# Kernel optimization log

Hardware: AMD Instinct MI355X
Metric: run time of the kernel (lower is better)

## Reference

```python
import jax, jax.numpy as jnp
import numpy as np

# Static DAG: input -> L hidden layers of K nodes (dense between layers) -> output.
B, WIDTH, K, L = 262144, 64, 4, 4


def _linear_init(key, shape, fan_in):
    # matches nn.Linear default: U(-1/sqrt(fan_in), 1/sqrt(fan_in))
    bound = 1.0 / np.sqrt(fan_in)
    return jax.random.uniform(key, shape, jnp.float32, -bound, bound)


def setup_inputs() -> dict:
    key = jax.random.key(0)
    ks = jax.random.split(key, 9)
    x = jax.random.normal(ks[0], (B, WIDTH), jnp.float32)
    # input node -> first hidden layer (K edges)
    W_in = _linear_init(ks[1], (K, WIDTH, WIDTH), WIDTH)
    b_in = _linear_init(ks[2], (K, WIDTH), WIDTH)
    # between hidden layers: (L-1) transitions, K*K edges each; [pred, node, out, in]
    W_mid = _linear_init(ks[3], (L - 1, K, K, WIDTH, WIDTH), WIDTH)
    b_mid = _linear_init(ks[4], (L - 1, K, K, WIDTH), WIDTH)
    # last hidden layer -> output node (K edges)
    W_out = _linear_init(ks[5], (K, WIDTH, WIDTH), WIDTH)
    b_out = _linear_init(ks[6], (K, WIDTH), WIDTH)
    return {"x": x, "W_in": W_in, "b_in": b_in, "W_mid": W_mid,
            "b_mid": b_mid, "W_out": W_out, "b_out": b_out}


def _l2_normalize(t):
    # torch.linalg.norm(t) with no dim: Frobenius norm over the WHOLE tensor
    return t / jnp.linalg.norm(t)


def reference(x, W_in, b_in, W_mid, b_mid, W_out, b_out):
    # input node -> layer 1: each node k gets a single edge Linear, then normalize
    h = jnp.einsum('bw,kvw->kbv', x, W_in) + b_in[:, None, :]  # [K,B,W]
    h = jax.vmap(_l2_normalize)(h)
    # hidden -> hidden transitions: node v sums over its K predecessor edges
    for l in range(L - 1):  # small fixed structural loop over layers
        pre = jnp.einsum('pbw,pkvw->kbv', h, W_mid[l]) + b_mid[l].sum(axis=0)[:, None, :]
        h = jax.vmap(_l2_normalize)(pre)
    # last layer -> output node: sum K edge outputs, normalize
    out = jnp.einsum('pbw,pvw->bv', h, W_out) + b_out.sum(axis=0)
    return _l2_normalize(out)
```

## Files before the change

kernel.cpp:

```cpp
#include <hip/hip_runtime.h>


#define BF 262144.0f
#define SLOT 4608

#define OFF_G   0
#define OFF_S   4096
#define OFF_P2  8192
#define OFF_C2  73728
#define OFF_P4  74752
#define OFF_C4  91136
#define OFF_MO  91392
#define OFF_CO  95488
#define OFF_X16 98304

typedef __attribute__((ext_vector_type(8))) short bf16x8;
typedef __attribute__((ext_vector_type(4))) float f32x4;
typedef __attribute__((ext_vector_type(4))) unsigned short u16x4;

__device__ __forceinline__ unsigned short f2bf(float f) {
  unsigned u = __builtin_bit_cast(unsigned, f);
  u += 0x7FFF + ((u >> 16) & 1);
  return (unsigned short)(u >> 16);
}
__device__ __forceinline__ float bf2f(unsigned short h) {
  unsigned u = ((unsigned)h) << 16;
  return __builtin_bit_cast(float, u);
}

__device__ __forceinline__ bf16x8 cvt8(f32x4 a, f32x4 b, float s) {
  bf16x8 t;
#pragma unroll
  for (int j = 0; j < 4; j++) {
    t[j]     = (short)f2bf(a[j] * s);
    t[j + 4] = (short)f2bf(b[j] * s);
  }
  return t;
}

__device__ __forceinline__ void split8(f32x4 a, f32x4 b, float sc,
                                       bf16x8& hi, bf16x8& lo) {
#pragma unroll
  for (int j = 0; j < 4; j++) {
    float v = a[j] * sc;
    unsigned short h = f2bf(v);
    hi[j] = (short)h; lo[j] = (short)f2bf(v - bf2f(h));
    v = b[j] * sc;
    h = f2bf(v);
    hi[j + 4] = (short)h; lo[j + 4] = (short)f2bf(v - bf2f(h));
  }
}

__device__ __forceinline__ float qpart(const unsigned short* th,
                                       const unsigned short* tl,
                                       int it, int col, int quad,
                                       const float Greg[4][4]) {
  f32x4 dq[4];
#pragma unroll
  for (int ut = 0; ut < 4; ut++) dq[ut] = (f32x4){0.f, 0.f, 0.f, 0.f};
#pragma unroll
  for (int ks = 0; ks < 2; ks++) {
    const bf16x8 ah = *(const bf16x8*)&th[(it * 16 + col) * 72 + ks * 32 + quad * 8];
    const bf16x8 al = *(const bf16x8*)&tl[(it * 16 + col) * 72 + ks * 32 + quad * 8];
#pragma unroll
    for (int ut = 0; ut < 4; ut++) {
      const bf16x8 bh = *(const bf16x8*)&th[(ut * 16 + col) * 72 + ks * 32 + quad * 8];
      const bf16x8 bl = *(const bf16x8*)&tl[(ut * 16 + col) * 72 + ks * 32 + quad * 8];
      dq[ut] = __builtin_amdgcn_mfma_f32_16x16x32_bf16(ah, bh, dq[ut], 0, 0, 0);
      dq[ut] = __builtin_amdgcn_mfma_f32_16x16x32_bf16(ah, bl, dq[ut], 0, 0, 0);
      dq[ut] = __builtin_amdgcn_mfma_f32_16x16x32_bf16(al, bh, dq[ut], 0, 0, 0);
    }
  }
  float qp = 0.f;
#pragma unroll
  for (int ut = 0; ut < 4; ut++)
#pragma unroll
    for (int r = 0; r < 4; r++) qp += dq[ut][r] * Greg[ut][r];
  return qp;
}

__device__ __forceinline__ void blkred(float qp, float* red4, float* qvv,
                                       int idx, int tid, int lane, int it) {
#pragma unroll
  for (int off = 32; off; off >>= 1) qp += __shfl_down(qp, off, 64);
  if (lane == 0) red4[it] = qp;
  __syncthreads();
  if (tid == 0) qvv[idx] = 1.0f / sqrtf(red4[0] + red4[1] + red4[2] + red4[3]);
  __syncthreads();
}

__global__ __launch_bounds__(256) void kG(const float* __restrict__ x,
                                          float* __restrict__ Gpart,
                                          unsigned short* __restrict__ x16) {
  __shared__ __align__(16) unsigned short xts[4][4][16][8];
  __shared__ float sred[256][4];
  const int tid = threadIdx.x;
  const int lane = tid & 63, mt = tid >> 6;
  const int col = lane & 15, q = lane >> 4;
  const int row0 = tid >> 4;
  const int cf0  = (tid & 15) * 4;

  f32x4 acc[4];
#pragma unroll
  for (int nt = 0; nt < 4; nt++) acc[nt] = (f32x4){0.f, 0.f, 0.f, 0.f};
  float s0 = 0.f, s1 = 0.f, s2 = 0.f, s3 = 0.f;

  const long brow = (long)blockIdx.x * 512;
  const float* bx = x + brow * 64;
  f32x4 r0 = *(const f32x4*)(bx + tid * 4);
  f32x4 r1 = *(const f32x4*)(bx + 1024 + tid * 4);

  for (int c = 0; c < 16; c++) {
    __syncthreads();
    s0 += r0[0] + r1[0]; s1 += r0[1] + r1[1];
    s2 += r0[2] + r1[2]; s3 += r0[3] + r1[3];
    u16x4 h0, h1;
#pragma unroll
    for (int j = 0; j < 4; j++) {
      const int cf = cf0 + j;
      const unsigned short b0 = f2bf(r0[j]);
      const unsigned short b1 = f2bf(r1[j]);
      h0[j] = b0; h1[j] = b1;
      xts[cf >> 4][row0 >> 3][cf & 15][row0 & 7]        = b0;
      xts[cf >> 4][2 + (row0 >> 3)][cf & 15][row0 & 7]  = b1;
    }
    *(u16x4*)(x16 + (brow + c * 32 + row0) * 64 + cf0)      = h0;
    *(u16x4*)(x16 + (brow + c * 32 + 16 + row0) * 64 + cf0) = h1;
    f32x4 r0n = r0, r1n = r1;
    if (c < 15) {
      r0n = *(const f32x4*)(bx + (c + 1) * 2048 + tid * 4);
      r1n = *(const f32x4*)(bx + (c + 1) * 2048 + 1024 + tid * 4);
    }
    __syncthreads();
    const bf16x8 af = *(const bf16x8*)xts[mt][q][col];
#pragma unroll
    for (int nt = 0; nt < 4; nt++) {
      const bf16x8 bfr = *(const bf16x8*)xts[nt][q][col];
      acc[nt] = __builtin_amdgcn_mfma_f32_16x16x32_bf16(af, bfr, acc[nt], 0, 0, 0);
    }
    r0 = r0n; r1 = r1n;
  }

  float* myp = Gpart + (long)blockIdx.x * 4160;
#pragma unroll
  for (int nt = 0; nt < 4; nt++)
#pragma unroll
    for (int r = 0; r < 4; r++)
      myp[(mt * 16 + q * 4 + r) * 64 + nt * 16 + col] = acc[nt][r];

  sred[tid][0] = s0; sred[tid][1] = s1; sred[tid][2] = s2; sred[tid][3] = s3;
  __syncthreads();
  if (tid < 64) {
    float t = 0.f;
#pragma unroll
    for (int k2 = 0; k2 < 16; k2++) t += sred[(tid >> 2) + 16 * k2][tid & 3];
    myp[4096 + tid] = t;
  }
}

__global__ __launch_bounds__(256) void kGred(const float* __restrict__ Gpart,
                                             float* __restrict__ G,
                                             float* __restrict__ s) {
  __shared__ float red[4][64];
  const int tid = threadIdx.x;
  const int e = blockIdx.x * 64 + (tid & 63);
  const int quarter = tid >> 6;
  float acc = 0.f;
#pragma unroll 4
  for (int j = 0; j < 128; j++)
    acc += Gpart[(long)(quarter * 128 + j) * 4160 + e];
  red[quarter][tid & 63] = acc;
  __syncthreads();
  if (tid < 64) {
    const float t = red[0][tid] + red[1][tid] + red[2][tid] + red[3][tid];
    const int ee = blockIdx.x * 64 + tid;
    if (ee < 4096) G[ee] = t;
    else           s[ee - 4096] = t;
  }
}

__global__ __launch_bounds__(256) void kChainA(
    const float* __restrict__ Win, const float* __restrict__ bin,
    const float* __restrict__ Wm0, const float* __restrict__ bm0,
    const float* __restrict__ Wm1, const float* __restrict__ bm1,
    const float* __restrict__ G, const float* __restrict__ s,
    float* __restrict__ Pout, float* __restrict__ cpout) {
  extern __shared__ __align__(16) char smem[];
  unsigned short* Tth = (unsigned short*)smem;
  unsigned short* Ttl = Tth + 4 * SLOT;
  float* cAv  = (float*)(Ttl + 4 * SLOT);
  float* cBv  = cAv + 256;
  float* slv  = cBv + 64;
  float* red4 = slv + 64;
  float* qvv  = red4 + 4;
  float* Tf   = qvv + 8;

  const int tid = threadIdx.x;
  const int p2 = blockIdx.x >> 2, k2 = blockIdx.x & 3;
  const int lane = tid & 63, it = tid >> 6;
  const int col = lane & 15, quad = lane >> 4;

  float Greg[4][4];
#pragma unroll
  for (int ut = 0; ut < 4; ut++)
#pragma unroll
    for (int r = 0; r < 4; r++)
      Greg[ut][r] = G[(it * 16 + quad * 4 + r) * 64 + ut * 16 + col];
  if (tid < 64) slv[tid] = s[tid];
  if (tid < 256) cAv[tid] = bin[tid];

  for (int p = 0; p < 4; p++) {
#pragma unroll
    for (int m = 0; m < 4; m++) {
      const int li = m * 1024 + tid * 4;
      *(f32x4*)&Tf[(li >> 6) * 68 + (li & 63)] = *(const f32x4*)(Win + p * 4096 + li);
    }
    __syncthreads();
    const int tc = tid >> 2, rb = (tid & 3) * 16;
#pragma unroll
    for (int j = 0; j < 16; j++) {
      const float tv = Tf[(rb + j) * 68 + tc];
      const unsigned short h = f2bf(tv);
      Tth[p * SLOT + tc * 72 + rb + j] = h;
      Ttl[p * SLOT + tc * 72 + rb + j] = f2bf(tv - bf2f(h));
    }
    __syncthreads();
  }

#pragma unroll
  for (int p = 0; p < 4; p++) {
    float qp = qpart(Tth + p * SLOT, Ttl + p * SLOT, it, col, quad, Greg);
    if (tid < 64) {
      float sd = 0.f;
      for (int w = 0; w < 64; w++)
        sd += slv[w] * (bf2f(Tth[p * SLOT + w * 72 + tid]) +
                        bf2f(Ttl[p * SLOT + w * 72 + tid]));
      const float c = cAv[p * 64 + tid];
      qp += c * (2.f * sd + BF * c);
    }
    blkred(qp, red4, qvv, p, tid, lane, it);
  }

  f32x4 dc[4];
#pragma unroll
  for (int nt = 0; nt < 4; nt++) dc[nt] = (f32x4){0.f, 0.f, 0.f, 0.f};
  float c2acc = 0.f;

  const int arow = it * 16 + col;
  f32x4 wr[4];
  {
    const float* wbase = Wm0 + (long)((0 * 4 + p2) * 64 + arow) * 64;
    wr[0] = *(const f32x4*)(wbase + quad * 8);
    wr[1] = *(const f32x4*)(wbase + quad * 8 + 4);
    wr[2] = *(const f32x4*)(wbase + 32 + quad * 8);
    wr[3] = *(const f32x4*)(wbase + 36 + quad * 8);
  }
#pragma unroll
  for (int p = 0; p < 4; p++) {
    const float inv = qvv[p];
    bf16x8 awh0, awl0, awh1, awl1;
    split8(wr[0], wr[1], inv, awh0, awl0);
    split8(wr[2], wr[3], inv, awh1, awl1);
    if (p < 3) {
      const float* wbase = Wm0 + (long)(((p + 1) * 4 + p2) * 64 + arow) * 64;
      wr[0] = *(const f32x4*)(wbase + quad * 8);
      wr[1] = *(const f32x4*)(wbase + quad * 8 + 4);
      wr[2] = *(const f32x4*)(wbase + 32 + quad * 8);
      wr[3] = *(const f32x4*)(wbase + 36 + quad * 8);
    }
#pragma unroll
    for (int nt = 0; nt < 4; nt++) {
      const bf16x8 bh0 = *(const bf16x8*)&Tth[p * SLOT + (nt * 16 + col) * 72 + quad * 8];
      const bf16x8 bl0 = *(const bf16x8*)&Ttl[p * SLOT + (nt * 16 + col) * 72 + quad * 8];
      dc[nt] = __builtin_amdgcn_mfma_f32_16x16x32_bf16(awh0, bh0, dc[nt], 0, 0, 0);
      dc[nt] = __builtin_amdgcn_mfma_f32_16x16x32_bf16(awh0, bl0, dc[nt], 0, 0, 0);
      dc[nt] = __builtin_amdgcn_mfma_f32_16x16x32_bf16(awl0, bh0, dc[nt], 0, 0, 0);
      const bf16x8 bh1 = *(const bf16x8*)&Tth[p * SLOT + (nt * 16 + col) * 72 + 32 + quad * 8];
      const bf16x8 bl1 = *(const bf16x8*)&Ttl[p * SLOT + (nt * 16 + col) * 72 + 32 + quad * 8];
      dc[nt] = __builtin_amdgcn_mfma_f32_16x16x32_bf16(awh1, bh1, dc[nt], 0, 0, 0);
      dc[nt] = __builtin_amdgcn_mfma_f32_16x16x32_bf16(awh1, bl1, dc[nt], 0, 0, 0);
      dc[nt] = __builtin_amdgcn_mfma_f32_16x16x32_bf16(awl1, bh1, dc[nt], 0, 0, 0);
    }
    if (tid < 64) {
      const float* wrow = Wm0 + (long)((p * 4 + p2) * 64 + tid) * 64;
      float pc = 0.f;
#pragma unroll
      for (int u4 = 0; u4 < 16; u4++) {
        const f32x4 wv = *(const f32x4*)(wrow + u4 * 4);
        pc += wv[0] * cAv[p * 64 + u4 * 4]     + wv[1] * cAv[p * 64 + u4 * 4 + 1] +
              wv[2] * cAv[p * 64 + u4 * 4 + 2] + wv[3] * cAv[p * 64 + u4 * 4 + 3];
      }
      c2acc += inv * pc + bm0[(p * 4 + p2) * 64 + tid];
    }
  }
  __syncthreads();

#pragma unroll
  for (int nt = 0; nt < 4; nt++)
#pragma unroll
    for (int r = 0; r < 4; r++) {
      const float val = dc[nt][r];
      const unsigned short h = f2bf(val);
      const int w_ = nt * 16 + col, v_ = it * 16 + quad * 4 + r;
      Tth[w_ * 72 + v_] = h;
      Ttl[w_ * 72 + v_] = f2bf(val - bf2f(h));
    }
  if (tid < 64) cBv[tid] = c2acc;
  __syncthreads();

  {
    float qp = qpart(Tth, Ttl, it, col, quad, Greg);
    if (tid < 64) {
      float sd = 0.f;
      for (int w = 0; w < 64; w++)
        sd += slv[w] * (bf2f(Tth[w * 72 + tid]) + bf2f(Ttl[w * 72 + tid]));
      const float c = cBv[tid];
      qp += c * (2.f * sd + BF * c);
    }
    blkred(qp, red4, qvv, 4, tid, lane, it);
  }
  const float inv2 = qvv[4];

  {
    f32x4 dcO[4];
#pragma unroll
    for (int nt = 0; nt < 4; nt++) dcO[nt] = (f32x4){0.f, 0.f, 0.f, 0.f};
    const float* wbase = Wm1 + (long)((p2 * 4 + k2) * 64 + arow) * 64;
    const f32x4 w0 = *(const f32x4*)(wbase + quad * 8);
    const f32x4 w1 = *(const f32x4*)(wbase + quad * 8 + 4);
    const f32x4 w2 = *(const f32x4*)(wbase + 32 + quad * 8);
    const f32x4 w3 = *(const f32x4*)(wbase + 36 + quad * 8);
    bf16x8 awh0, awl0, awh1, awl1;
    split8(w0, w1, inv2, awh0, awl0);
    split8(w2, w3, inv2, awh1, awl1);
#pragma unroll
    for (int nt = 0; nt < 4; nt++) {
      const bf16x8 bh0 = *(const bf16x8*)&Tth[(nt * 16 + col) * 72 + quad * 8];
      const bf16x8 bl0 = *(const bf16x8*)&Ttl[(nt * 16 + col) * 72 + quad * 8];
      dcO[nt] = __builtin_amdgcn_mfma_f32_16x16x32_bf16(awh0, bh0, dcO[nt], 0, 0, 0);
      dcO[nt] = __builtin_amdgcn_mfma_f32_16x16x32_bf16(awh0, bl0, dcO[nt], 0, 0, 0);
      dcO[nt] = __builtin_amdgcn_mfma_f32_16x16x32_bf16(awl0, bh0, dcO[nt], 0, 0, 0);
      const bf16x8 bh1 = *(const bf16x8*)&Tth[(nt * 16 + col) * 72 + 32 + quad * 8];
      const bf16x8 bl1 = *(const bf16x8*)&Ttl[(nt * 16 + col) * 72 + 32 + quad * 8];
      dcO[nt] = __builtin_amdgcn_mfma_f32_16x16x32_bf16(awh1, bh1, dcO[nt], 0, 0, 0);
      dcO[nt] = __builtin_amdgcn_mfma_f32_16x16x32_bf16(awh1, bl1, dcO[nt], 0, 0, 0);
      dcO[nt] = __builtin_amdgcn_mfma_f32_16x16x32_bf16(awl1, bh1, dcO[nt], 0, 0, 0);
    }
    float* po = Pout + (long)(p2 * 4 + k2) * 4096;
#pragma unroll
    for (int nt = 0; nt < 4; nt++)
#pragma unroll
      for (int r = 0; r < 4; r++)
        po[(it * 16 + quad * 4 + r) * 64 + nt * 16 + col] = dcO[nt][r];
    if (tid < 64) {
      const float* wrow = Wm1 + (long)((p2 * 4 + k2) * 64 + tid) * 64;
      float pc = 0.f;
#pragma unroll
      for (int u4 = 0; u4 < 16; u4++) {
        const f32x4 wv = *(const f32x4*)(wrow + u4 * 4);
        pc += wv[0] * cBv[u4 * 4]     + wv[1] * cBv[u4 * 4 + 1] +
              wv[2] * cBv[u4 * 4 + 2] + wv[3] * cBv[u4 * 4 + 3];
      }
      cpout[(p2 * 4 + k2) * 64 + tid] = inv2 * pc + bm1[(p2 * 4 + k2) * 64 + tid];
    }
  }
}

__global__ __launch_bounds__(256) void kChainB(
    const float* __restrict__ Pin, const float* __restrict__ cpin,
    const float* __restrict__ Wm2, const float* __restrict__ bm2,
    const float* __restrict__ Wout, const float* __restrict__ bout,
    const float* __restrict__ G, const float* __restrict__ s,
    float* __restrict__ Pout, float* __restrict__ cpout) {
  extern __shared__ __align__(16) char smem[];
  unsigned short* Tth = (unsigned short*)smem;
  unsigned short* Ttl = Tth + 4 * SLOT;
  float* cAv  = (float*)(Ttl + 4 * SLOT);
  float* cBv  = cAv + 256;
  float* slv  = cBv + 64;
  float* red4 = slv + 64;
  float* qvv  = red4 + 4;
  float* Tf   = qvv + 8;

  const int tid = threadIdx.x;
  const int kp = blockIdx.x;
  const int lane = tid & 63, it = tid >> 6;
  const int col = lane & 15, quad = lane >> 4;

  float Greg[4][4];
#pragma unroll
  for (int ut = 0; ut < 4; ut++)
#pragma unroll
    for (int r = 0; r < 4; r++)
      Greg[ut][r] = G[(it * 16 + quad * 4 + r) * 64 + ut * 16 + col];
  if (tid < 64) slv[tid] = s[tid];
  if (tid < 256) {
    const int k = tid >> 6, v = tid & 63;
    cAv[tid] = cpin[(0 * 4 + k) * 64 + v] + cpin[(1 * 4 + k) * 64 + v] +
               cpin[(2 * 4 + k) * 64 + v] + cpin[(3 * 4 + k) * 64 + v];
  }

  for (int k = 0; k < 4; k++) {
#pragma unroll
    for (int m = 0; m < 4; m++) {
      const int li = m * 1024 + tid * 4;
      const f32x4 a = *(const f32x4*)(Pin + (0 * 4 + k) * 4096 + li);
      const f32x4 b = *(const f32x4*)(Pin + (1 * 4 + k) * 4096 + li);
      const f32x4 c = *(const f32x4*)(Pin + (2 * 4 + k) * 4096 + li);
      const f32x4 d = *(const f32x4*)(Pin + (3 * 4 + k) * 4096 + li);
      *(f32x4*)&Tf[(li >> 6) * 68 + (li & 63)] = a + b + c + d;
    }
    __syncthreads();
    const int tc = tid >> 2, rb = (tid & 3) * 16;
#pragma unroll
    for (int j = 0; j < 16; j++) {
      const float tv = Tf[(rb + j) * 68 + tc];
      const unsigned short h = f2bf(tv);
      Tth[k * SLOT + tc * 72 + rb + j] = h;
      Ttl[k * SLOT + tc * 72 + rb + j] = f2bf(tv - bf2f(h));
    }
    __syncthreads();
  }

#pragma unroll
  for (int k = 0; k < 4; k++) {
    float qp = qpart(Tth + k * SLOT, Ttl + k * SLOT, it, col, quad, Greg);
    if (tid < 64) {
      float sd = 0.f;
      for (int w = 0; w < 64; w++)
        sd += slv[w] * (bf2f(Tth[k * SLOT + w * 72 + tid]) +
                        bf2f(Ttl[k * SLOT + w * 72 + tid]));
      const float c = cAv[k * 64 + tid];
      qp += c * (2.f * sd + BF * c);
    }
    blkred(qp, red4, qvv, k, tid, lane, it);
  }

  f32x4 dc[4];
#pragma unroll
  for (int nt = 0; nt < 4; nt++) dc[nt] = (f32x4){0.f, 0.f, 0.f, 0.f};
  float c4acc = 0.f;

  const int arow = it * 16 + col;
  f32x4 wr[4];
  {
    const float* wbase = Wm2 + (long)((0 * 4 + kp) * 64 + arow) * 64;
    wr[0] = *(const f32x4*)(wbase + quad * 8);
    wr[1] = *(const f32x4*)(wbase + quad * 8 + 4);
    wr[2] = *(const f32x4*)(wbase + 32 + quad * 8);
    wr[3] = *(const f32x4*)(wbase + 36 + quad * 8);
  }
#pragma unroll
  for (int k = 0; k < 4; k++) {
    const float inv = qvv[k];
    bf16x8 awh0, awl0, awh1, awl1;
    split8(wr[0], wr[1], inv, awh0, awl0);
    split8(wr[2], wr[3], inv, awh1, awl1);
    if (k < 3) {
      const float* wbase = Wm2 + (long)(((k + 1) * 4 + kp) * 64 + arow) * 64;
      wr[0] = *(const f32x4*)(wbase + quad * 8);
      wr[1] = *(const f32x4*)(wbase + quad * 8 + 4);
      wr[2] = *(const f32x4*)(wbase + 32 + quad * 8);
      wr[3] = *(const f32x4*)(wbase + 36 + quad * 8);
    }
#pragma unroll
    for (int nt = 0; nt < 4; nt++) {
      const bf16x8 bh0 = *(const bf16x8*)&Tth[k * SLOT + (nt * 16 + col) * 72 + quad * 8];
      const bf16x8 bl0 = *(const bf16x8*)&Ttl[k * SLOT + (nt * 16 + col) * 72 + quad * 8];
      dc[nt] = __builtin_amdgcn_mfma_f32_16x16x32_bf16(awh0, bh0, dc[nt], 0, 0, 0);
      dc[nt] = __builtin_amdgcn_mfma_f32_16x16x32_bf16(awh0, bl0, dc[nt], 0, 0, 0);
      dc[nt] = __builtin_amdgcn_mfma_f32_16x16x32_bf16(awl0, bh0, dc[nt], 0, 0, 0);
      const bf16x8 bh1 = *(const bf16x8*)&Tth[k * SLOT + (nt * 16 + col) * 72 + 32 + quad * 8];
      const bf16x8 bl1 = *(const bf16x8*)&Ttl[k * SLOT + (nt * 16 + col) * 72 + 32 + quad * 8];
      dc[nt] = __builtin_amdgcn_mfma_f32_16x16x32_bf16(awh1, bh1, dc[nt], 0, 0, 0);
      dc[nt] = __builtin_amdgcn_mfma_f32_16x16x32_bf16(awh1, bl1, dc[nt], 0, 0, 0);
      dc[nt] = __builtin_amdgcn_mfma_f32_16x16x32_bf16(awl1, bh1, dc[nt], 0, 0, 0);
    }
    if (tid < 64) {
      const float* wrow = Wm2 + (long)((k * 4 + kp) * 64 + tid) * 64;
      float pc = 0.f;
#pragma unroll
      for (int u4 = 0; u4 < 16; u4++) {
        const f32x4 wv = *(const f32x4*)(wrow + u4 * 4);
        pc += wv[0] * cAv[k * 64 + u4 * 4]     + wv[1] * cAv[k * 64 + u4 * 4 + 1] +
              wv[2] * cAv[k * 64 + u4 * 4 + 2] + wv[3] * cAv[k * 64 + u4 * 4 + 3];
      }
      c4acc += inv * pc + bm2[(k * 4 + kp) * 64 + tid];
    }
  }
  __syncthreads();

#pragma unroll
  for (int nt = 0; nt < 4; nt++)
#pragma unroll
    for (int r = 0; r < 4; r++) {
      const float val = dc[nt][r];
      const unsigned short h = f2bf(val);
      const int w_ = nt * 16 + col, v_ = it * 16 + quad * 4 + r;
      Tth[w_ * 72 + v_] = h;
      Ttl[w_ * 72 + v_] = f2bf(val - bf2f(h));
    }
  if (tid < 64) cBv[tid] = c4acc;
  __syncthreads();

  {
    float qp = qpart(Tth, Ttl, it, col, quad, Greg);
    if (tid < 64) {
      float sd = 0.f;
      for (int w = 0; w < 64; w++)
        sd += slv[w] * (bf2f(Tth[w * 72 + tid]) + bf2f(Ttl[w * 72 + tid]));
      const float c = cBv[tid];
      qp += c * (2.f * sd + BF * c);
    }
    blkred(qp, red4, qvv, 4, tid, lane, it);
  }
  const float inv4 = qvv[4];

  {
    f32x4 dcO[4];
#pragma unroll
    for (int nt = 0; nt < 4; nt++) dcO[nt] = (f32x4){0.f, 0.f, 0.f, 0.f};
    const float* wbase = Wout + (long)(kp * 64 + arow) * 64;
    const f32x4 w0 = *(const f32x4*)(wbase + quad * 8);
    const f32x4 w1 = *(const f32x4*)(wbase + quad * 8 + 4);
    const f32x4 w2 = *(const f32x4*)(wbase + 32 + quad * 8);
    const f32x4 w3 = *(const f32x4*)(wbase + 36 + quad * 8);
    bf16x8 awh0, awl0, awh1, awl1;
    split8(w0, w1, inv4, awh0, awl0);
    split8(w2, w3, inv4, awh1, awl1);
#pragma unroll
    for (int nt = 0; nt < 4; nt++) {
      const bf16x8 bh0 = *(const bf16x8*)&Tth[(nt * 16 + col) * 72 + quad * 8];
      const bf16x8 bl0 = *(const bf16x8*)&Ttl[(nt * 16 + col) * 72 + quad * 8];
      dcO[nt] = __builtin_amdgcn_mfma_f32_16x16x32_bf16(awh0, bh0, dcO[nt], 0, 0, 0);
      dcO[nt] = __builtin_amdgcn_mfma_f32_16x16x32_bf16(awh0, bl0, dcO[nt], 0, 0, 0);
      dcO[nt] = __builtin_amdgcn_mfma_f32_16x16x32_bf16(awl0, bh0, dcO[nt], 0, 0, 0);
      const bf16x8 bh1 = *(const bf16x8*)&Tth[(nt * 16 + col) * 72 + 32 + quad * 8];
      const bf16x8 bl1 = *(const bf16x8*)&Ttl[(nt * 16 + col) * 72 + 32 + quad * 8];
      dcO[nt] = __builtin_amdgcn_mfma_f32_16x16x32_bf16(awh1, bh1, dcO[nt], 0, 0, 0);
      dcO[nt] = __builtin_amdgcn_mfma_f32_16x16x32_bf16(awh1, bl1, dcO[nt], 0, 0, 0);
      dcO[nt] = __builtin_amdgcn_mfma_f32_16x16x32_bf16(awl1, bh1, dcO[nt], 0, 0, 0);
    }
    float* po = Pout + (long)kp * 4096;
#pragma unroll
    for (int nt = 0; nt < 4; nt++)
#pragma unroll
      for (int r = 0; r < 4; r++)
        po[(it * 16 + quad * 4 + r) * 64 + nt * 16 + col] = dcO[nt][r];
    if (tid < 64) {
      const float* wrow = Wout + (long)(kp * 64 + tid) * 64;
      float pc = 0.f;
#pragma unroll
      for (int u4 = 0; u4 < 16; u4++) {
        const f32x4 wv = *(const f32x4*)(wrow + u4 * 4);
        pc += wv[0] * cBv[u4 * 4]     + wv[1] * cBv[u4 * 4 + 1] +
              wv[2] * cBv[u4 * 4 + 2] + wv[3] * cBv[u4 * 4 + 3];
      }
      cpout[kp * 64 + tid] = inv4 * pc + bout[kp * 64 + tid];
    }
  }
}

__global__ __launch_bounds__(256) void kNorm(const float* __restrict__ Psrc,
                                             const float* __restrict__ csrc,
                                             const float* __restrict__ G,
                                             const float* __restrict__ s,
                                             float* __restrict__ MoS,
                                             float* __restrict__ coS) {
  __shared__ float Tf[64][68];
  __shared__ __align__(16) unsigned short Tth[64][68], Ttl[64][68];
  __shared__ float red[256];
  __shared__ __align__(16) float cl[64], sl[64];
  const int tid = threadIdx.x;
  const int lane = tid & 63, it = tid >> 6;
  const int col = lane & 15, quad = lane >> 4;

  float Greg[4][4];
#pragma unroll
  for (int ut = 0; ut < 4; ut++)
#pragma unroll
    for (int r = 0; r < 4; r++)
      Greg[ut][r] = G[(it * 16 + quad * 4 + r) * 64 + ut * 16 + col];

#pragma unroll
  for (int m = 0; m < 16; m++) {
    const int li = m * 256 + tid;
    Tf[li >> 6][li & 63] = Psrc[li] + Psrc[4096 + li] + Psrc[8192 + li] + Psrc[12288 + li];
  }
  if (tid < 64) {
    cl[tid] = csrc[tid] + csrc[64 + tid] + csrc[128 + tid] + csrc[192 + tid];
    sl[tid] = s[tid];
  }
  __syncthreads();

  {
    const int tc = tid >> 2;
    const int rb = (tid & 3) * 16;
#pragma unroll
    for (int j = 0; j < 16; j++) {
      const float tv = Tf[rb + j][tc];
      const unsigned short h = f2bf(tv);
      Tth[tc][rb + j] = h;
      Ttl[tc][rb + j] = f2bf(tv - bf2f(h));
    }
  }
  __syncthreads();

  float qp = 0.f;
  {
    f32x4 dq[4];
#pragma unroll
    for (int ut = 0; ut < 4; ut++) dq[ut] = (f32x4){0.f, 0.f, 0.f, 0.f};
#pragma unroll
    for (int ks = 0; ks < 2; ks++) {
      const bf16x8 ah = *(const bf16x8*)&Tth[it * 16 + col][ks * 32 + quad * 8];
      const bf16x8 al = *(const bf16x8*)&Ttl[it * 16 + col][ks * 32 + quad * 8];
#pragma unroll
      for (int ut = 0; ut < 4; ut++) {
        const bf16x8 bh = *(const bf16x8*)&Tth[ut * 16 + col][ks * 32 + quad * 8];
        const bf16x8 bl = *(const bf16x8*)&Ttl[ut * 16 + col][ks * 32 + quad * 8];
        dq[ut] = __builtin_amdgcn_mfma_f32_16x16x32_bf16(ah, bh, dq[ut], 0, 0, 0);
        dq[ut] = __builtin_amdgcn_mfma_f32_16x16x32_bf16(ah, bl, dq[ut], 0, 0, 0);
        dq[ut] = __builtin_amdgcn_mfma_f32_16x16x32_bf16(al, bh, dq[ut], 0, 0, 0);
      }
    }
#pragma unroll
    for (int ut = 0; ut < 4; ut++)
#pragma unroll
      for (int r = 0; r < 4; r++)
        qp += dq[ut][r] * Greg[ut][r];
  }
  if (tid < 64) {
    float sd = 0.f;
#pragma unroll
    for (int u4 = 0; u4 < 16; u4++) {
      const f32x4 tv = *(const f32x4*)&Tf[tid][u4 * 4];
      const f32x4 sv = *(const f32x4*)&sl[u4 * 4];
      sd += sv[0] * tv[0] + sv[1] * tv[1] + sv[2] * tv[2] + sv[3] * tv[3];
    }
    qp += cl[tid] * (2.f * sd + BF * cl[tid]);
  }
  red[tid] = qp;
  __syncthreads();
  for (int st = 128; st > 0; st >>= 1) {
    if (tid < st) red[tid] += red[tid + st];
    __syncthreads();
  }
  const float inv = 1.0f / sqrtf(red[0]);

#pragma unroll
  for (int m = 0; m < 16; m++) {
    const int li = m * 256 + tid;
    MoS[li] = inv * Tf[li >> 6][li & 63];
  }
  if (tid < 64) coS[tid] = inv * cl[tid];
}

__global__ __launch_bounds__(256) void kApply(const unsigned short* __restrict__ x16,
                                              const float* __restrict__ MoS,
                                              const float* __restrict__ coS,
                                              float* __restrict__ out) {
  const int tid = threadIdx.x, lane = tid & 63, vt = tid >> 6;
  const int col = lane & 15, q = lane >> 4;

  bf16x8 bfr[2];
  const float* mr = MoS + (vt * 16 + col) * 64 + q * 8;
  bfr[0] = cvt8(*(const f32x4*)mr, *(const f32x4*)(mr + 4), 1.f);
  bfr[1] = cvt8(*(const f32x4*)(mr + 32), *(const f32x4*)(mr + 36), 1.f);
  const float cf = coS[vt * 16 + col];

  for (int t = 0; t < 16; t++) {
    const int b0 = (blockIdx.x * 16 + t) * 16;
    const unsigned short* xr = x16 + (long)(b0 + col) * 64 + q * 8;
    const bf16x8 a0 = *(const bf16x8*)xr;
    const bf16x8 a1 = *(const bf16x8*)(xr + 32);
    f32x4 acc = (f32x4){0.f, 0.f, 0.f, 0.f};
    acc = __builtin_amdgcn_mfma_f32_16x16x32_bf16(a0, bfr[0], acc, 0, 0, 0);
    acc = __builtin_amdgcn_mfma_f32_16x16x32_bf16(a1, bfr[1], acc, 0, 0, 0);
#pragma unroll
    for (int r = 0; r < 4; r++)
      out[(long)(b0 + q * 4 + r) * 64 + vt * 16 + col] = acc[r] + cf;
  }
}

extern "C" void kernel_launch(void* const* d_in, const int* in_sizes, int n_in,
                              void* d_out, int out_size, void* d_ws, size_t ws_size,
                              hipStream_t stream) {
  const float* x    = (const float*)d_in[0];
  const float* Win  = (const float*)d_in[1];
  const float* bin  = (const float*)d_in[2];
  const float* Wmid = (const float*)d_in[3];
  const float* bmid = (const float*)d_in[4];
  const float* Wout = (const float*)d_in[5];
  const float* bout = (const float*)d_in[6];
  float* out = (float*)d_out;
  float* ws  = (float*)d_ws;
  float* Gpart = out;
  unsigned short* x16 = (unsigned short*)(ws + OFF_X16);

  const size_t SMEM = (size_t)(8 * SLOT) * 2 + (396 + 8 + 64 * 68) * 4 + 64;
  hipFuncSetAttribute((const void*)kChainA,
                      hipFuncAttributeMaxDynamicSharedMemorySize, (int)SMEM);
  hipFuncSetAttribute((const void*)kChainB,
                      hipFuncAttributeMaxDynamicSharedMemorySize, (int)SMEM);

  kG   <<<512, 256, 0, stream>>>(x, Gpart, x16);
  kGred<<<65, 256, 0, stream>>>(Gpart, ws + OFF_G, ws + OFF_S);
  kChainA<<<16, 256, SMEM, stream>>>(Win, bin, Wmid, bmid, Wmid + 65536, bmid + 1024,
                                     ws + OFF_G, ws + OFF_S, ws + OFF_P2, ws + OFF_C2);
  kChainB<<<4, 256, SMEM, stream>>>(ws + OFF_P2, ws + OFF_C2,
                                    Wmid + 131072, bmid + 2048, Wout, bout,
                                    ws + OFF_G, ws + OFF_S, ws + OFF_P4, ws + OFF_C4);
  kNorm<<<1, 256, 0, stream>>>(ws + OFF_P4, ws + OFF_C4, ws + OFF_G, ws + OFF_S,
                               ws + OFF_MO, ws + OFF_CO);
  kApply<<<1024, 256, 0, stream>>>(x16, ws + OFF_MO, ws + OFF_CO, out);
}
```

Baseline: 226.8 us.

## Fuse weight-chain composition kernels into a single one-block kernel

Replaces the kChainA (16 blocks), kChainB (4 blocks) and kNorm launches with one single-block kernel. That kernel composes all layer weight matrices and norms sequentially in shared memory, ping-ponging between two split-bf16 buffers. This removes two kernel launches and the global round-trips for the partial products. In exchange, the full composition runs serially on one CU where it was previously spread over up to 16 blocks, so the chain's critical path may grow.

```diff
diff --git a/kernel.cpp b/kernel.cpp
--- a/kernel.cpp
+++ b/kernel.cpp
@@ -6,10 +6,6 @@
 
 #define OFF_G   0
 #define OFF_S   4096
-#define OFF_P2  8192
-#define OFF_C2  73728
-#define OFF_P4  74752
-#define OFF_C4  91136
 #define OFF_MO  91392
 #define OFF_CO  95488
 #define OFF_X16 98304
@@ -86,6 +82,108 @@
   if (lane == 0) red4[it] = qp;
   __syncthreads();
   if (tid == 0) qvv[idx] = 1.0f / sqrtf(red4[0] + red4[1] + red4[2] + red4[3]);
+  __syncthreads();
+}
+
+__device__ __forceinline__ void qphase(const unsigned short* th0,
+                                       const unsigned short* tl0,
+                                       const float* cX, const float Greg[4][4],
+                                       const float* slv, float* red4, float* qvv,
+                                       int tid, int lane, int it, int col, int quad) {
+#pragma unroll
+  for (int n = 0; n < 4; n++) {
+    float qp = qpart(th0 + n * SLOT, tl0 + n * SLOT, it, col, quad, Greg);
+    if (tid < 64) {
+      float sd = 0.f;
+      for (int w = 0; w < 64; w++)
+        sd += slv[w] * (bf2f(th0[n * SLOT + w * 72 + tid]) +
+                        bf2f(tl0[n * SLOT + w * 72 + tid]));
+      const float c = cX[n * 64 + tid];
+      qp += c * (2.f * sd + BF * c);
+    }
+    blkred(qp, red4, qvv, n, tid, lane, it);
+  }
+}
+
+__device__ __forceinline__ void compose(const unsigned short* sTh, const unsigned short* sTl,
+                                        unsigned short* dTh, unsigned short* dTl,
+                                        const float* cSrc, float* cDst,
+                                        const float* Wl, const float* bl,
+                                        const float* qvv,
+                                        int tid, int lane, int it, int col, int quad) {
+  const int arow = it * 16 + col;
+  f32x4 wr[4];
+  {
+    const float* wbase = Wl + (long)(0 * 64 + arow) * 64;
+    wr[0] = *(const f32x4*)(wbase + quad * 8);
+    wr[1] = *(const f32x4*)(wbase + quad * 8 + 4);
+    wr[2] = *(const f32x4*)(wbase + 32 + quad * 8);
+    wr[3] = *(const f32x4*)(wbase + 36 + quad * 8);
+  }
+  f32x4 dc[4];
+#pragma unroll
+  for (int nt = 0; nt < 4; nt++) dc[nt] = (f32x4){0.f, 0.f, 0.f, 0.f};
+#pragma unroll
+  for (int e = 0; e < 16; e++) {
+    const int tgt = e >> 2, src = e & 3;
+    const float inv = qvv[src];
+    bf16x8 awh0, awl0, awh1, awl1;
+    split8(wr[0], wr[1], inv, awh0, awl0);
+    split8(wr[2], wr[3], inv, awh1, awl1);
+    if (e < 15) {
+      const int e1 = e + 1, tgt1 = e1 >> 2, src1 = e1 & 3;
+      const float* wbase = Wl + (long)((src1 * 4 + tgt1) * 64 + arow) * 64;
+      wr[0] = *(const f32x4*)(wbase + quad * 8);
+      wr[1] = *(const f32x4*)(wbase + quad * 8 + 4);
+      wr[2] = *(const f32x4*)(wbase + 32 + quad * 8);
+      wr[3] = *(const f32x4*)(wbase + 36 + quad * 8);
+    }
+    const unsigned short* bh_ = sTh + src * SLOT;
+    const unsigned short* bl_ = sTl + src * SLOT;
+#pragma unroll
+    for (int nt = 0; nt < 4; nt++) {
+      const bf16x8 bh0 = *(const bf16x8*)&bh_[(nt * 16 + col) * 72 + quad * 8];
+      const bf16x8 bl0 = *(const bf16x8*)&bl_[(nt * 16 + col) * 72 + quad * 8];
+      dc[nt] = __builtin_amdgcn_mfma_f32_16x16x32_bf16(awh0, bh0, dc[nt], 0, 0, 0);
+      dc[nt] = __builtin_amdgcn_mfma_f32_16x16x32_bf16(awh0, bl0, dc[nt], 0, 0, 0);
+      dc[nt] = __builtin_amdgcn_mfma_f32_16x16x32_bf16(awl0, bh0, dc[nt], 0, 0, 0);
+      const bf16x8 bh1 = *(const bf16x8*)&bh_[(nt * 16 + col) * 72 + 32 + quad * 8];
+      const bf16x8 bl1 = *(const bf16x8*)&bl_[(nt * 16 + col) * 72 + 32 + quad * 8];
+      dc[nt] = __builtin_amdgcn_mfma_f32_16x16x32_bf16(awh1, bh1, dc[nt], 0, 0, 0);
+      dc[nt] = __builtin_amdgcn_mfma_f32_16x16x32_bf16(awh1, bl1, dc[nt], 0, 0, 0);
+      dc[nt] = __builtin_amdgcn_mfma_f32_16x16x32_bf16(awl1, bh1, dc[nt], 0, 0, 0);
+    }
+    if (src == 3) {
+#pragma unroll
+      for (int nt = 0; nt < 4; nt++)
+#pragma unroll
+        for (int r = 0; r < 4; r++) {
+          const float val = dc[nt][r];
+          const unsigned short h = f2bf(val);
+          const int w_ = nt * 16 + col, v_ = it * 16 + quad * 4 + r;
+          dTh[tgt * SLOT + w_ * 72 + v_] = h;
+          dTl[tgt * SLOT + w_ * 72 + v_] = f2bf(val - bf2f(h));
+        }
+#pragma unroll
+      for (int nt = 0; nt < 4; nt++) dc[nt] = (f32x4){0.f, 0.f, 0.f, 0.f};
+    }
+  }
+  {
+    float acc = 0.f;
+#pragma unroll
+    for (int src = 0; src < 4; src++) {
+      const float* wrow = Wl + (long)((src * 4 + it) * 64 + lane) * 64;
+      float pc = 0.f;
+#pragma unroll
+      for (int u4 = 0; u4 < 16; u4++) {
+        const f32x4 wv = *(const f32x4*)(wrow + u4 * 4);
+        pc += wv[0] * cSrc[src * 64 + u4 * 4]     + wv[1] * cSrc[src * 64 + u4 * 4 + 1] +
+              wv[2] * cSrc[src * 64 + u4 * 4 + 2] + wv[3] * cSrc[src * 64 + u4 * 4 + 3];
+      }
+      acc += qvv[src] * pc + bl[(src * 4 + it) * 64 + lane];
+    }
+    cDst[it * 64 + lane] = acc;
+  }
   __syncthreads();
 }
 
@@ -179,24 +277,29 @@
   }
 }
 
-__global__ __launch_bounds__(256) void kChainA(
+__global__ __launch_bounds__(256) void kChain1(
     const float* __restrict__ Win, const float* __restrict__ bin,
-    const float* __restrict__ Wm0, const float* __restrict__ bm0,
-    const float* __restrict__ Wm1, const float* __restrict__ bm1,
+    const float* __restrict__ Wmid, const float* __restrict__ bmid,
+    const float* __restrict__ Wout, const float* __restrict__ bout,
     const float* __restrict__ G, const float* __restrict__ s,
-    float* __restrict__ Pout, float* __restrict__ cpout) {
+    float* __restrict__ MoS, float* __restrict__ coS) {
   extern __shared__ __align__(16) char smem[];
-  unsigned short* Tth = (unsigned short*)smem;
-  unsigned short* Ttl = Tth + 4 * SLOT;
-  float* cAv  = (float*)(Ttl + 4 * SLOT);
-  float* cBv  = cAv + 256;
-  float* slv  = cBv + 64;
+  unsigned short* ThA = (unsigned short*)smem;
+  unsigned short* TlA = ThA + 4 * SLOT;
+  unsigned short* ThB = TlA + 4 * SLOT;
+  unsigned short* TlB = ThB + 4 * SLOT;
+  float* cA   = (float*)(TlB + 4 * SLOT);
+  float* cB   = cA + 256;
+  float* cF   = cB + 256;
+  float* slv  = cF + 64;
   float* red4 = slv + 64;
   float* qvv  = red4 + 4;
-  float* Tf   = qvv + 8;
+
+  const float* Wm0 = Wmid;            const float* bm0 = bmid;
+  const float* Wm1 = Wmid + 65536;    const float* bm1 = bmid + 1024;
+  const float* Wm2 = Wmid + 131072;   const float* bm2 = bmid + 2048;
 
   const int tid = threadIdx.x;
-  const int p2 = blockIdx.x >> 2, k2 = blockIdx.x & 3;
   const int lane = tid & 63, it = tid >> 6;
   const int col = lane & 15, quad = lane >> 4;
 
@@ -207,453 +310,127 @@
     for (int r = 0; r < 4; r++)
       Greg[ut][r] = G[(it * 16 + quad * 4 + r) * 64 + ut * 16 + col];
   if (tid < 64) slv[tid] = s[tid];
-  if (tid < 256) cAv[tid] = bin[tid];
-
-  for (int p = 0; p < 4; p++) {
-#pragma unroll
-    for (int m = 0; m < 4; m++) {
-      const int li = m * 1024 + tid * 4;
-      *(f32x4*)&Tf[(li >> 6) * 68 + (li & 63)] = *(const f32x4*)(Win + p * 4096 + li);
-    }
-    __syncthreads();
-    const int tc = tid >> 2, rb = (tid & 3) * 16;
-#pragma unroll
-    for (int j = 0; j < 16; j++) {
-      const float tv = Tf[(rb + j) * 68 + tc];
-      const unsigned short h = f2bf(tv);
-      Tth[p * SLOT + tc * 72 + rb + j] = h;
-      Ttl[p * SLOT + tc * 72 + rb + j] = f2bf(tv - bf2f(h));
-    }
-    __syncthreads();
-  }
-
-#pragma unroll
-  for (int p = 0; p < 4; p++) {
-    float qp = qpart(Tth + p * SLOT, Ttl + p * SLOT, it, col, quad, Greg);
-    if (tid < 64) {
-      float sd = 0.f;
-      for (int w = 0; w < 64; w++)
-        sd += slv[w] * (bf2f(Tth[p * SLOT + w * 72 + tid]) +
-                        bf2f(Ttl[p * SLOT + w * 72 + tid]));
-      const float c = cAv[p * 64 + tid];
-      qp += c * (2.f * sd + BF * c);
-    }
-    blkred(qp, red4, qvv, p, tid, lane, it);
-  }
-
-  f32x4 dc[4];
-#pragma unroll
-  for (int nt = 0; nt < 4; nt++) dc[nt] = (f32x4){0.f, 0.f, 0.f, 0.f};
-  float c2acc = 0.f;
-
-  const int arow = it * 16 + col;
-  f32x4 wr[4];
+  cA[tid] = bin[tid];
+
   {
-    const float* wbase = Wm0 + (long)((0 * 4 + p2) * 64 + arow) * 64;
-    wr[0] = *(const f32x4*)(wbase + quad * 8);
-    wr[1] = *(const f32x4*)(wbase + quad * 8 + 4);
-    wr[2] = *(const f32x4*)(wbase + 32 + quad * 8);
-    wr[3] = *(const f32x4*)(wbase + 36 + quad * 8);
-  }
-#pragma unroll
-  for (int p = 0; p < 4; p++) {
-    const float inv = qvv[p];
-    bf16x8 awh0, awl0, awh1, awl1;
-    split8(wr[0], wr[1], inv, awh0, awl0);
-    split8(wr[2], wr[3], inv, awh1, awl1);
-    if (p < 3) {
-      const float* wbase = Wm0 + (long)(((p + 1) * 4 + p2) * 64 + arow) * 64;
+    float* Tf = (float*)ThB;
+    for (int p = 0; p < 4; p++) {
+#pragma unroll
+      for (int m = 0; m < 4; m++) {
+        const int li = m * 1024 + tid * 4;
+        *(f32x4*)&Tf[(li >> 6) * 68 + (li & 63)] = *(const f32x4*)(Win + p * 4096 + li);
+      }
+      __syncthreads();
+      const int tc = tid >> 2, rb = (tid & 3) * 16;
+#pragma unroll
+      for (int j = 0; j < 16; j++) {
+        const float tv = Tf[(rb + j) * 68 + tc];
+        const unsigned short h = f2bf(tv);
+        ThA[p * SLOT + tc * 72 + rb + j] = h;
+        TlA[p * SLOT + tc * 72 + rb + j] = f2bf(tv - bf2f(h));
+      }
+      __syncthreads();
+    }
+  }
+
+  qphase(ThA, TlA, cA, Greg, slv, red4, qvv, tid, lane, it, col, quad);
+  compose(ThA, TlA, ThB, TlB, cA, cB, Wm0, bm0, qvv, tid, lane, it, col, quad);
+  qphase(ThB, TlB, cB, Greg, slv, red4, qvv, tid, lane, it, col, quad);
+  compose(ThB, TlB, ThA, TlA, cB, cA, Wm1, bm1, qvv, tid, lane, it, col, quad);
+  qphase(ThA, TlA, cA, Greg, slv, red4, qvv, tid, lane, it, col, quad);
+  compose(ThA, TlA, ThB, TlB, cA, cB, Wm2, bm2, qvv, tid, lane, it, col, quad);
+  qphase(ThB, TlB, cB, Greg, slv, red4, qvv, tid, lane, it, col, quad);
+
+  {
+    const int arow = it * 16 + col;
+    f32x4 dcF[4];
+#pragma unroll
+    for (int nt = 0; nt < 4; nt++) dcF[nt] = (f32x4){0.f, 0.f, 0.f, 0.f};
+    f32x4 wr[4];
+    {
+      const float* wbase = Wout + (long)(0 * 64 + arow) * 64;
       wr[0] = *(const f32x4*)(wbase + quad * 8);
       wr[1] = *(const f32x4*)(wbase + quad * 8 + 4);
       wr[2] = *(const f32x4*)(wbase + 32 + quad * 8);
       wr[3] = *(const f32x4*)(wbase + 36 + quad * 8);
     }
 #pragma unroll
-    for (int nt = 0; nt < 4; nt++) {
-      const bf16x8 bh0 = *(const bf16x8*)&Tth[p * SLOT + (nt * 16 + col) * 72 + quad * 8];
-      const bf16x8 bl0 = *(const bf16x8*)&Ttl[p * SLOT + (nt * 16 + col) * 72 + quad * 8];
-      dc[nt] = __builtin_amdgcn_mfma_f32_16x16x32_bf16(awh0, bh0, dc[nt], 0, 0, 0);
-      dc[nt] = __builtin_amdgcn_mfma_f32_16x16x32_bf16(awh0, bl0, dc[nt], 0, 0, 0);
-      dc[nt] = __builtin_amdgcn_mfma_f32_16x16x32_bf16(awl0, bh0, dc[nt], 0, 0, 0);
-      const bf16x8 bh1 = *(const bf16x8*)&Tth[p * SLOT + (nt * 16 + col) * 72 + 32 + quad * 8];
-      const bf16x8 bl1 = *(const bf16x8*)&Ttl[p * SLOT + (nt * 16 + col) * 72 + 32 + quad * 8];
-      dc[nt] = __builtin_amdgcn_mfma_f32_16x16x32_bf16(awh1, bh1, dc[nt], 0, 0, 0);
-      dc[nt] = __builtin_amdgcn_mfma_f32_16x16x32_bf16(awh1, bl1, dc[nt], 0, 0, 0);
-      dc[nt] = __builtin_amdgcn_mfma_f32_16x16x32_bf16(awl1, bh1, dc[nt], 0, 0, 0);
-    }
-    if (tid < 64) {
-      const float* wrow = Wm0 + (long)((p * 4 + p2) * 64 + tid) * 64;
+    for (int kp = 0; kp < 4; kp++) {
+      const float inv = qvv[kp];
+      bf16x8 awh0, awl0, awh1, awl1;
+      split8(wr[0], wr[1], inv, awh0, awl0);
+      split8(wr[2], wr[3], inv, awh1, awl1);
+      if (kp < 3) {
+        const float* wbase = Wout + (long)((kp + 1) * 64 + arow) * 64;
+        wr[0] = *(const f32x4*)(wbase + quad * 8);
+        wr[1] = *(const f32x4*)(wbase + quad * 8 + 4);
+        wr[2] = *(const f32x4*)(wbase + 32 + quad * 8);
+        wr[3] = *(const f32x4*)(wbase + 36 + quad * 8);
+      }
+#pragma unroll
+      for (int nt = 0; nt < 4; nt++) {
+        const bf16x8 bh0 = *(const bf16x8*)&ThB[kp * SLOT + (nt * 16 + col) * 72 + quad * 8];
+        const bf16x8 bl0 = *(const bf16x8*)&TlB[kp * SLOT + (nt * 16 + col) * 72 + quad * 8];
+        dcF[nt] = __builtin_amdgcn_mfma_f32_16x16x32_bf16(awh0, bh0, dcF[nt], 0, 0, 0);
+        dcF[nt] = __builtin_amdgcn_mfma_f32_16x16x32_bf16(awh0, bl0, dcF[nt], 0, 0, 0);
+        dcF[nt] = __builtin_amdgcn_mfma_f32_16x16x32_bf16(awl0, bh0, dcF[nt], 0, 0, 0);
+        const bf16x8 bh1 = *(const bf16x8*)&ThB[kp * SLOT + (nt * 16 + col) * 72 + 32 + quad * 8];
+        const bf16x8 bl1 = *(const bf16x8*)&TlB[kp * SLOT + (nt * 16 + col) * 72 + 32 + quad * 8];
+        dcF[nt] = __builtin_amdgcn_mfma_f32_16x16x32_bf16(awh1, bh1, dcF[nt], 0, 0, 0);
+        dcF[nt] = __builtin_amdgcn_mfma_f32_16x16x32_bf16(awh1, bl1, dcF[nt], 0, 0, 0);
+        dcF[nt] = __builtin_amdgcn_mfma_f32_16x16x32_bf16(awl1, bh1, dcF[nt], 0, 0, 0);
+      }
+    }
+    {
+      const float* wrow = Wout + (long)(it * 64 + lane) * 64;
       float pc = 0.f;
 #pragma unroll
       for (int u4 = 0; u4 < 16; u4++) {
         const f32x4 wv = *(const f32x4*)(wrow + u4 * 4);
-        pc += wv[0] * cAv[p * 64 + u4 * 4]     + wv[1] * cAv[p * 64 + u4 * 4 + 1] +
-              wv[2] * cAv[p * 64 + u4 * 4 + 2] + wv[3] * cAv[p * 64 + u4 * 4 + 3];
-      }
-      c2acc += inv * pc + bm0[(p * 4 + p2) * 64 + tid];
-    }
-  }
-  __syncthreads();
-
-#pragma unroll
-  for (int nt = 0; nt < 4; nt++)
-#pragma unroll
-    for (int r = 0; r < 4; r++) {
-      const float val = dc[nt][r];
-      const unsigned short h = f2bf(val);
-      const int w_ = nt * 16 + col, v_ = it * 16 + quad * 4 + r;
-      Tth[w_ * 72 + v_] = h;
-      Ttl[w_ * 72 + v_] = f2bf(val - bf2f(h));
-    }
-  if (tid < 64) cBv[tid] = c2acc;
-  __syncthreads();
-
-  {
-    float qp = qpart(Tth, Ttl, it, col, quad, Greg);
+        pc += wv[0] * cB[it * 64 + u4 * 4]     + wv[1] * cB[it * 64 + u4 * 4 + 1] +
+              wv[2] * cB[it * 64 + u4 * 4 + 2] + wv[3] * cB[it * 64 + u4 * 4 + 3];
+      }
+      cA[it * 64 + lane] = qvv[it] * pc + bout[it * 64 + lane];
+    }
+    float* TfF = (float*)ThA;
+    unsigned short* Th2 = ThA + 2 * SLOT;
+    unsigned short* Tl2 = TlA + 2 * SLOT;
+#pragma unroll
+    for (int nt = 0; nt < 4; nt++)
+#pragma unroll
+      for (int r = 0; r < 4; r++) {
+        const float val = dcF[nt][r];
+        const int v_ = it * 16 + quad * 4 + r, w_ = nt * 16 + col;
+        TfF[v_ * 68 + w_] = val;
+        const unsigned short h = f2bf(val);
+        Th2[w_ * 72 + v_] = h;
+        Tl2[w_ * 72 + v_] = f2bf(val - bf2f(h));
+      }
+    __syncthreads();
+    if (tid < 64) cF[tid] = cA[tid] + cA[64 + tid] + cA[128 + tid] + cA[192 + tid];
+    __syncthreads();
+
+    float qp = qpart(Th2, Tl2, it, col, quad, Greg);
     if (tid < 64) {
       float sd = 0.f;
-      for (int w = 0; w < 64; w++)
-        sd += slv[w] * (bf2f(Tth[w * 72 + tid]) + bf2f(Ttl[w * 72 + tid]));
-      const float c = cBv[tid];
-      qp += c * (2.f * sd + BF * c);
+#pragma unroll
+      for (int u4 = 0; u4 < 16; u4++) {
+        const f32x4 tv = *(const f32x4*)&TfF[tid * 68 + u4 * 4];
+        const f32x4 sv = *(const f32x4*)&slv[u4 * 4];
+        sd += sv[0] * tv[0] + sv[1] * tv[1] + sv[2] * tv[2] + sv[3] * tv[3];
+      }
+      qp += cF[tid] * (2.f * sd + BF * cF[tid]);
     }
     blkred(qp, red4, qvv, 4, tid, lane, it);
-  }
-  const float inv2 = qvv[4];
-
-  {
-    f32x4 dcO[4];
-#pragma unroll
-    for (int nt = 0; nt < 4; nt++) dcO[nt] = (f32x4){0.f, 0.f, 0.f, 0.f};
-    const float* wbase = Wm1 + (long)((p2 * 4 + k2) * 64 + arow) * 64;
-    const f32x4 w0 = *(const f32x4*)(wbase + quad * 8);
-    const f32x4 w1 = *(const f32x4*)(wbase + quad * 8 + 4);
-    const f32x4 w2 = *(const f32x4*)(wbase + 32 + quad * 8);
-    const f32x4 w3 = *(const f32x4*)(wbase + 36 + quad * 8);
-    bf16x8 awh0, awl0, awh1, awl1;
-    split8(w0, w1, inv2, awh0, awl0);
-    split8(w2, w3, inv2, awh1, awl1);
-#pragma unroll
-    for (int nt = 0; nt < 4; nt++) {
-      const bf16x8 bh0 = *(const bf16x8*)&Tth[(nt * 16 + col) * 72 + quad * 8];
-      const bf16x8 bl0 = *(const bf16x8*)&Ttl[(nt * 16 + col) * 72 + quad * 8];
-      dcO[nt] = __builtin_amdgcn_mfma_f32_16x16x32_bf16(awh0, bh0, dcO[nt], 0, 0, 0);
-      dcO[nt] = __builtin_amdgcn_mfma_f32_16x16x32_bf16(awh0, bl0, dcO[nt], 0, 0, 0);
-      dcO[nt] = __builtin_amdgcn_mfma_f32_16x16x32_bf16(awl0, bh0, dcO[nt], 0, 0, 0);
-      const bf16x8 bh1 = *(const bf16x8*)&Tth[(nt * 16 + col) * 72 + 32 + quad * 8];
-      const bf16x8 bl1 = *(const bf16x8*)&Ttl[(nt * 16 + col) * 72 + 32 + quad * 8];
-      dcO[nt] = __builtin_amdgcn_mfma_f32_16x16x32_bf16(awh1, bh1, dcO[nt], 0, 0, 0);
-      dcO[nt] = __builtin_amdgcn_mfma_f32_16x16x32_bf16(awh1, bl1, dcO[nt], 0, 0, 0);
-      dcO[nt] = __builtin_amdgcn_mfma_f32_16x16x32_bf16(awl1, bh1, dcO[nt], 0, 0, 0);
-    }
-    float* po = Pout + (long)(p2 * 4 + k2) * 4096;
-#pragma unroll
-    for (int nt = 0; nt < 4; nt++)
-#pragma unroll
-      for (int r = 0; r < 4; r++)
-        po[(it * 16 + quad * 4 + r) * 64 + nt * 16 + col] = dcO[nt][r];
-    if (tid < 64) {
-      const float* wrow = Wm1 + (long)((p2 * 4 + k2) * 64 + tid) * 64;
-      float pc = 0.f;
-#pragma unroll
-      for (int u4 = 0; u4 < 16; u4++) {
-        const f32x4 wv = *(const f32x4*)(wrow + u4 * 4);
-        pc += wv[0] * cBv[u4 * 4]     + wv[1] * cBv[u4 * 4 + 1] +
-              wv[2] * cBv[u4 * 4 + 2] + wv[3] * cBv[u4 * 4 + 3];
-      }
-      cpout[(p2 * 4 + k2) * 64 + tid] = inv2 * pc + bm1[(p2 * 4 + k2) * 64 + tid];
-    }
-  }
-}
-
-__global__ __launch_bounds__(256) void kChainB(
-    const float* __restrict__ Pin, const float* __restrict__ cpin,
-    const float* __restrict__ Wm2, const float* __restrict__ bm2,
-    const float* __restrict__ Wout, const float* __restrict__ bout,
-    const float* __restrict__ G, const float* __restrict__ s,
-    float* __restrict__ Pout, float* __restrict__ cpout) {
-  extern __shared__ __align__(16) char smem[];
-  unsigned short* Tth = (unsigned short*)smem;
-  unsigned short* Ttl = Tth + 4 * SLOT;
-  float* cAv  = (float*)(Ttl + 4 * SLOT);
-  float* cBv  = cAv + 256;
-  float* slv  = cBv + 64;
-  float* red4 = slv + 64;
-  float* qvv  = red4 + 4;
-  float* Tf   = qvv + 8;
-
-  const int tid = threadIdx.x;
-  const int kp = blockIdx.x;
-  const int lane = tid & 63, it = tid >> 6;
-  const int col = lane & 15, quad = lane >> 4;
-
-  float Greg[4][4];
-#pragma unroll
-  for (int ut = 0; ut < 4; ut++)
-#pragma unroll
-    for (int r = 0; r < 4; r++)
-      Greg[ut][r] = G[(it * 16 + quad * 4 + r) * 64 + ut * 16 + col];
-  if (tid < 64) slv[tid] = s[tid];
-  if (tid < 256) {
-    const int k = tid >> 6, v = tid & 63;
-    cAv[tid] = cpin[(0 * 4 + k) * 64 + v] + cpin[(1 * 4 + k) * 64 + v] +
-               cpin[(2 * 4 + k) * 64 + v] + cpin[(3 * 4 + k) * 64 + v];
-  }
-
-  for (int k = 0; k < 4; k++) {
-#pragma unroll
-    for (int m = 0; m < 4; m++) {
-      const int li = m * 1024 + tid * 4;
-      const f32x4 a = *(const f32x4*)(Pin + (0 * 4 + k) * 4096 + li);
-      const f32x4 b = *(const f32x4*)(Pin + (1 * 4 + k) * 4096 + li);
-      const f32x4 c = *(const f32x4*)(Pin + (2 * 4 + k) * 4096 + li);
-      const f32x4 d = *(const f32x4*)(Pin + (3 * 4 + k) * 4096 + li);
-      *(f32x4*)&Tf[(li >> 6) * 68 + (li & 63)] = a + b + c + d;
-    }
-    __syncthreads();
-    const int tc = tid >> 2, rb = (tid & 3) * 16;
-#pragma unroll
-    for (int j = 0; j < 16; j++) {
-      const float tv = Tf[(rb + j) * 68 + tc];
-      const unsigned short h = f2bf(tv);
-      Tth[k * SLOT + tc * 72 + rb + j] = h;
-      Ttl[k * SLOT + tc * 72 + rb + j] = f2bf(tv - bf2f(h));
-    }
-    __syncthreads();
-  }
-
-#pragma unroll
-  for (int k = 0; k < 4; k++) {
-    float qp = qpart(Tth + k * SLOT, Ttl + k * SLOT, it, col, quad, Greg);
-    if (tid < 64) {
-      float sd = 0.f;
-      for (int w = 0; w < 64; w++)
-        sd += slv[w] * (bf2f(Tth[k * SLOT + w * 72 + tid]) +
-                        bf2f(Ttl[k * SLOT + w * 72 + tid]));
-      const float c = cAv[k * 64 + tid];
-      qp += c * (2.f * sd + BF * c);
-    }
-    blkred(qp, red4, qvv, k, tid, lane, it);
-  }
-
-  f32x4 dc[4];
-#pragma unroll
-  for (int nt = 0; nt < 4; nt++) dc[nt] = (f32x4){0.f, 0.f, 0.f, 0.f};
-  float c4acc = 0.f;
-
-  const int arow = it * 16 + col;
-  f32x4 wr[4];
-  {
-    const float* wbase = Wm2 + (long)((0 * 4 + kp) * 64 + arow) * 64;
-    wr[0] = *(const f32x4*)(wbase + quad * 8);
-    wr[1] = *(const f32x4*)(wbase + quad * 8 + 4);
-    wr[2] = *(const f32x4*)(wbase + 32 + quad * 8);
-    wr[3] = *(const f32x4*)(wbase + 36 + quad * 8);
-  }
-#pragma unroll
-  for (int k = 0; k < 4; k++) {
-    const float inv = qvv[k];
-    bf16x8 awh0, awl0, awh1, awl1;
-    split8(wr[0], wr[1], inv, awh0, awl0);
-    split8(wr[2], wr[3], inv, awh1, awl1);
-    if (k < 3) {
-      const float* wbase = Wm2 + (long)(((k + 1) * 4 + kp) * 64 + arow) * 64;
-      wr[0] = *(const f32x4*)(wbase + quad * 8);
-      wr[1] = *(const f32x4*)(wbase + quad * 8 + 4);
-      wr[2] = *(const f32x4*)(wbase + 32 + quad * 8);
-      wr[3] = *(const f32x4*)(wbase + 36 + quad * 8);
-    }
-#pragma unroll
-    for (int nt = 0; nt < 4; nt++) {
-      const bf16x8 bh0 = *(const bf16x8*)&Tth[k * SLOT + (nt * 16 + col) * 72 + quad * 8];
-      const bf16x8 bl0 = *(const bf16x8*)&Ttl[k * SLOT + (nt * 16 + col) * 72 + quad * 8];
-      dc[nt] = __builtin_amdgcn_mfma_f32_16x16x32_bf16(awh0, bh0, dc[nt], 0, 0, 0);
-      dc[nt] = __builtin_amdgcn_mfma_f32_16x16x32_bf16(awh0, bl0, dc[nt], 0, 0, 0);
-      dc[nt] = __builtin_amdgcn_mfma_f32_16x16x32_bf16(awl0, bh0, dc[nt], 0, 0, 0);
-      const bf16x8 bh1 = *(const bf16x8*)&Tth[k * SLOT + (nt * 16 + col) * 72 + 32 + quad * 8];
-      const bf16x8 bl1 = *(const bf16x8*)&Ttl[k * SLOT + (nt * 16 + col) * 72 + 32 + quad * 8];
-      dc[nt] = __builtin_amdgcn_mfma_f32_16x16x32_bf16(awh1, bh1, dc[nt], 0, 0, 0);
-      dc[nt] = __builtin_amdgcn_mfma_f32_16x16x32_bf16(awh1, bl1, dc[nt], 0, 0, 0);
-      dc[nt] = __builtin_amdgcn_mfma_f32_16x16x32_bf16(awl1, bh1, dc[nt], 0, 0, 0);
-    }
-    if (tid < 64) {
-      const float* wrow = Wm2 + (long)((k * 4 + kp) * 64 + tid) * 64;
-      float pc = 0.f;
-#pragma unroll
-      for (int u4 = 0; u4 < 16; u4++) {
-        const f32x4 wv = *(const f32x4*)(wrow + u4 * 4);
-        pc += wv[0] * cAv[k * 64 + u4 * 4]     + wv[1] * cAv[k * 64 + u4 * 4 + 1] +
-              wv[2] * cAv[k * 64 + u4 * 4 + 2] + wv[3] * cAv[k * 64 + u4 * 4 + 3];
-      }
-      c4acc += inv * pc + bm2[(k * 4 + kp) * 64 + tid];
-    }
-  }
-  __syncthreads();
-
-#pragma unroll
-  for (int nt = 0; nt < 4; nt++)
-#pragma unroll
-    for (int r = 0; r < 4; r++) {
-      const float val = dc[nt][r];
-      const unsigned short h = f2bf(val);
-      const int w_ = nt * 16 + col, v_ = it * 16 + quad * 4 + r;
-      Tth[w_ * 72 + v_] = h;
-      Ttl[w_ * 72 + v_] = f2bf(val - bf2f(h));
-    }
-  if (tid < 64) cBv[tid] = c4acc;
-  __syncthreads();
-
-  {
-    float qp = qpart(Tth, Ttl, it, col, quad, Greg);
-    if (tid < 64) {
-      float sd = 0.f;
-      for (int w = 0; w < 64; w++)
-        sd += slv[w] * (bf2f(Tth[w * 72 + tid]) + bf2f(Ttl[w * 72 + tid]));
-      const float c = cBv[tid];
-      qp += c * (2.f * sd + BF * c);
-    }
-    blkred(qp, red4, qvv, 4, tid, lane, it);
-  }
-  const float inv4 = qvv[4];
-
-  {
-    f32x4 dcO[4];
-#pragma unroll
-    for (int nt = 0; nt < 4; nt++) dcO[nt] = (f32x4){0.f, 0.f, 0.f, 0.f};
-    const float* wbase = Wout + (long)(kp * 64 + arow) * 64;
-    const f32x4 w0 = *(const f32x4*)(wbase + quad * 8);
-    const f32x4 w1 = *(const f32x4*)(wbase + quad * 8 + 4);
-    const f32x4 w2 = *(const f32x4*)(wbase + 32 + quad * 8);
-    const f32x4 w3 = *(const f32x4*)(wbase + 36 + quad * 8);
-    bf16x8 awh0, awl0, awh1, awl1;
-    split8(w0, w1, inv4, awh0, awl0);
-    split8(w2, w3, inv4, awh1, awl1);
-#pragma unroll
-    for (int nt = 0; nt < 4; nt++) {
-      const bf16x8 bh0 = *(const bf16x8*)&Tth[(nt * 16 + col) * 72 + quad * 8];
-      const bf16x8 bl0 = *(const bf16x8*)&Ttl[(nt * 16 + col) * 72 + quad * 8];
-      dcO[nt] = __builtin_amdgcn_mfma_f32_16x16x32_bf16(awh0, bh0, dcO[nt], 0, 0, 0);
-      dcO[nt] = __builtin_amdgcn_mfma_f32_16x16x32_bf16(awh0, bl0, dcO[nt], 0, 0, 0);
-      dcO[nt] = __builtin_amdgcn_mfma_f32_16x16x32_bf16(awl0, bh0, dcO[nt], 0, 0, 0);
-      const bf16x8 bh1 = *(const bf16x8*)&Tth[(nt * 16 + col) * 72 + 32 + quad * 8];
-      const bf16x8 bl1 = *(const bf16x8*)&Ttl[(nt * 16 + col) * 72 + 32 + quad * 8];
-      dcO[nt] = __builtin_amdgcn_mfma_f32_16x16x32_bf16(awh1, bh1, dcO[nt], 0, 0, 0);
-      dcO[nt] = __builtin_amdgcn_mfma_f32_16x16x32_bf16(awh1, bl1, dcO[nt], 0, 0, 0);
-      dcO[nt] = __builtin_amdgcn_mfma_f32_16x16x32_bf16(awl1, bh1, dcO[nt], 0, 0, 0);
-    }
-    float* po = Pout + (long)kp * 4096;
-#pragma unroll
-    for (int nt = 0; nt < 4; nt++)
-#pragma unroll
-      for (int r = 0; r < 4; r++)
-        po[(it * 16 + quad * 4 + r) * 64 + nt * 16 + col] = dcO[nt][r];
-    if (tid < 64) {
-      const float* wrow = Wout + (long)(kp * 64 + tid) * 64;
-      float pc = 0.f;
-#pragma unroll
-      for (int u4 = 0; u4 < 16; u4++) {
-        const f32x4 wv = *(const f32x4*)(wrow + u4 * 4);
-        pc += wv[0] * cBv[u4 * 4]     + wv[1] * cBv[u4 * 4 + 1] +
-              wv[2] * cBv[u4 * 4 + 2] + wv[3] * cBv[u4 * 4 + 3];
-      }
-      cpout[kp * 64 + tid] = inv4 * pc + bout[kp * 64 + tid];
-    }
-  }
-}
-
-__global__ __launch_bounds__(256) void kNorm(const float* __restrict__ Psrc,
-                                             const float* __restrict__ csrc,
-                                             const float* __restrict__ G,
-                                             const float* __restrict__ s,
-                                             float* __restrict__ MoS,
-                                             float* __restrict__ coS) {
-  __shared__ float Tf[64][68];
-  __shared__ __align__(16) unsigned short Tth[64][68], Ttl[64][68];
-  __shared__ float red[256];
-  __shared__ __align__(16) float cl[64], sl[64];
-  const int tid = threadIdx.x;
-  const int lane = tid & 63, it = tid >> 6;
-  const int col = lane & 15, quad = lane >> 4;
-
-  float Greg[4][4];
-#pragma unroll
-  for (int ut = 0; ut < 4; ut++)
-#pragma unroll
-    for (int r = 0; r < 4; r++)
-      Greg[ut][r] = G[(it * 16 + quad * 4 + r) * 64 + ut * 16 + col];
-
-#pragma unroll
-  for (int m = 0; m < 16; m++) {
-    const int li = m * 256 + tid;
-    Tf[li >> 6][li & 63] = Psrc[li] + Psrc[4096 + li] + Psrc[8192 + li] + Psrc[12288 + li];
-  }
-  if (tid < 64) {
-    cl[tid] = csrc[tid] + csrc[64 + tid] + csrc[128 + tid] + csrc[192 + tid];
-    sl[tid] = s[tid];
-  }
-  __syncthreads();
-
-  {
-    const int tc = tid >> 2;
-    const int rb = (tid & 3) * 16;
-#pragma unroll
-    for (int j = 0; j < 16; j++) {
-      const float tv = Tf[rb + j][tc];
-      const unsigned short h = f2bf(tv);
-      Tth[tc][rb + j] = h;
-      Ttl[tc][rb + j] = f2bf(tv - bf2f(h));
-    }
-  }
-  __syncthreads();
-
-  float qp = 0.f;
-  {
-    f32x4 dq[4];
-#pragma unroll
-    for (int ut = 0; ut < 4; ut++) dq[ut] = (f32x4){0.f, 0.f, 0.f, 0.f};
-#pragma unroll
-    for (int ks = 0; ks < 2; ks++) {
-      const bf16x8 ah = *(const bf16x8*)&Tth[it * 16 + col][ks * 32 + quad * 8];
-      const bf16x8 al = *(const bf16x8*)&Ttl[it * 16 + col][ks * 32 + quad * 8];
-#pragma unroll
-      for (int ut = 0; ut < 4; ut++) {
-        const bf16x8 bh = *(const bf16x8*)&Tth[ut * 16 + col][ks * 32 + quad * 8];
-        const bf16x8 bl = *(const bf16x8*)&Ttl[ut * 16 + col][ks * 32 + quad * 8];
-        dq[ut] = __builtin_amdgcn_mfma_f32_16x16x32_bf16(ah, bh, dq[ut], 0, 0, 0);
-        dq[ut] = __builtin_amdgcn_mfma_f32_16x16x32_bf16(ah, bl, dq[ut], 0, 0, 0);
-        dq[ut] = __builtin_amdgcn_mfma_f32_16x16x32_bf16(al, bh, dq[ut], 0, 0, 0);
-      }
-    }
-#pragma unroll
-    for (int ut = 0; ut < 4; ut++)
-#pragma unroll
-      for (int r = 0; r < 4; r++)
-        qp += dq[ut][r] * Greg[ut][r];
-  }
-  if (tid < 64) {
-    float sd = 0.f;
-#pragma unroll
-    for (int u4 = 0; u4 < 16; u4++) {
-      const f32x4 tv = *(const f32x4*)&Tf[tid][u4 * 4];
-      const f32x4 sv = *(const f32x4*)&sl[u4 * 4];
-      sd += sv[0] * tv[0] + sv[1] * tv[1] + sv[2] * tv[2] + sv[3] * tv[3];
-    }
-    qp += cl[tid] * (2.f * sd + BF * cl[tid]);
-  }
-  red[tid] = qp;
-  __syncthreads();
-  for (int st = 128; st > 0; st >>= 1) {
-    if (tid < st) red[tid] += red[tid + st];
-    __syncthreads();
-  }
-  const float inv = 1.0f / sqrtf(red[0]);
-
-#pragma unroll
-  for (int m = 0; m < 16; m++) {
-    const int li = m * 256 + tid;
-    MoS[li] = inv * Tf[li >> 6][li & 63];
-  }
-  if (tid < 64) coS[tid] = inv * cl[tid];
+    const float inv = qvv[4];
+
+#pragma unroll
+    for (int m = 0; m < 16; m++) {
+      const int li = m * 256 + tid;
+      MoS[li] = inv * TfF[(li >> 6) * 68 + (li & 63)];
+    }
+    if (tid < 64) coS[tid] = inv * cF[tid];
+  }
 }
 
 __global__ __launch_bounds__(256) void kApply(const unsigned short* __restrict__ x16,
@@ -698,20 +475,14 @@
   float* Gpart = out;
   unsigned short* x16 = (unsigned short*)(ws + OFF_X16);
 
-  const size_t SMEM = (size_t)(8 * SLOT) * 2 + (396 + 8 + 64 * 68) * 4 + 64;
-  hipFuncSetAttribute((const void*)kChainA,
-                      hipFuncAttributeMaxDynamicSharedMemorySize, (int)SMEM);
-  hipFuncSetAttribute((const void*)kChainB,
-                      hipFuncAttributeMaxDynamicSharedMemorySize, (int)SMEM);
+  const size_t SMEM2 = (size_t)(16 * SLOT) * 2 + 652 * 4;
+  hipFuncSetAttribute((const void*)kChain1,
+                      hipFuncAttributeMaxDynamicSharedMemorySize, (int)SMEM2);
 
   kG   <<<512, 256, 0, stream>>>(x, Gpart, x16);
   kGred<<<65, 256, 0, stream>>>(Gpart, ws + OFF_G, ws + OFF_S);
-  kChainA<<<16, 256, SMEM, stream>>>(Win, bin, Wmid, bmid, Wmid + 65536, bmid + 1024,
-                                     ws + OFF_G, ws + OFF_S, ws + OFF_P2, ws + OFF_C2);
-  kChainB<<<4, 256, SMEM, stream>>>(ws + OFF_P2, ws + OFF_C2,
-                                    Wmid + 131072, bmid + 2048, Wout, bout,
-                                    ws + OFF_G, ws + OFF_S, ws + OFF_P4, ws + OFF_C4);
-  kNorm<<<1, 256, 0, stream>>>(ws + OFF_P4, ws + OFF_C4, ws + OFF_G, ws + OFF_S,
-                               ws + OFF_MO, ws + OFF_CO);
+  kChain1<<<1, 256, SMEM2, stream>>>(Win, bin, Wmid, bmid, Wout, bout,
+                                     ws + OFF_G, ws + OFF_S,
+                                     ws + OFF_MO, ws + OFF_CO);
   kApply<<<1024, 256, 0, stream>>>(x16, ws + OFF_MO, ws + OFF_CO, out);
 }
```

New measurement: 292.2 us. 1.29x slower.
